# Optimization experiments

Measured on AMD Instinct MI355X. Metric: run time of the kernel, lower is better.

## Reference

```python
import jax, jax.numpy as jnp
import numpy as np

N = 50000   # num entities
R2 = 480    # num_rels * 2
D = 200     # h_dim
T = 4       # sequence_len (graph snapshots)
E = 100000  # edges per snapshot
L = 2       # rgcn layers
SLOPE = (1.0 / 8.0 + 1.0 / 3.0) / 2.0  # deterministic rrelu (eval-mode expected slope)


def setup_inputs() -> dict:
    key = jax.random.key(0)
    ks = jax.random.split(key, 13)
    s = 1.0 / np.sqrt(D)
    w = lambda k, shp, sc: jax.random.normal(k, shp, dtype=jnp.float32) * sc
    return {
        "src": jax.random.randint(ks[0], (T, E), 0, N, dtype=jnp.int32),
        "dst": jax.random.randint(ks[1], (T, E), 0, N, dtype=jnp.int32),
        "etype": jax.random.randint(ks[2], (T, E), 0, R2, dtype=jnp.int32),
        "dynamic_emb": w(ks[3], (N, D), 1.0),
        "emb_rel": w(ks[4], (R2, D), s),
        "W_ih": w(ks[5], (3 * D, 2 * D), s),
        "W_hh": w(ks[6], (3 * D, D), s),
        "b_ih": jnp.zeros((3 * D,), jnp.float32),
        "b_hh": jnp.zeros((3 * D,), jnp.float32),
        "W_neighbor": w(ks[7], (L, D, D), s),
        "W_loop": w(ks[8], (L, D, D), s),
        "time_gate_weight": w(ks[9], (D, D), s),
        "time_gate_bias": jnp.zeros((D,), jnp.float32),
    }


def _l2norm(x):
    n = jnp.linalg.norm(x, axis=-1, keepdims=True)
    return x / jnp.maximum(n, 1e-12)


def _gru(x, hprev, W_ih, W_hh, b_ih, b_hh):
    gi = x @ W_ih.T + b_ih
    gh = hprev @ W_hh.T + b_hh
    ir, iz, inn = jnp.split(gi, 3, axis=-1)
    hr, hz, hn = jnp.split(gh, 3, axis=-1)
    r = jax.nn.sigmoid(ir + hr)
    z = jax.nn.sigmoid(iz + hz)
    n = jnp.tanh(inn + r * hn)
    return (1.0 - z) * n + z * hprev


def reference(src, dst, etype, dynamic_emb, emb_rel, W_ih, W_hh, b_ih, b_hh,
              W_neighbor, W_loop, time_gate_weight, time_gate_bias):
    h_init = _l2norm(dynamic_emb)  # layer_norm=True path (F.normalize)

    def step(carry, g):
        h, h0 = carry
        s, d_, et = g
        # per-relation mean of entity embeddings touching that relation (r_to_e spans)
        ent_idx = jnp.concatenate([s, d_])          # [2E]
        seg = jnp.concatenate([et, et])             # [2E]
        ssum = jax.ops.segment_sum(h[ent_idx], seg, num_segments=R2)
        cnt = jax.ops.segment_sum(jnp.ones_like(seg, jnp.float32), seg, num_segments=R2)
        x_mean = ssum / jnp.maximum(cnt, 1.0)[:, None]          # absent rels stay 0
        x_input = jnp.concatenate([emb_rel, x_mean], axis=1)    # [R2, 2D]
        h0 = _l2norm(_gru(x_input, h0, W_ih, W_hh, b_ih, b_hh))
        # UnionRGCNLayer x L: gather -> sum-aggregate -> norm + self-loop -> rrelu
        deg = jax.ops.segment_sum(jnp.ones_like(d_, jnp.float32), d_, num_segments=N)
        norm = 1.0 / jnp.maximum(deg, 1.0)
        hh = h
        for l in range(L):
            pre = hh[s] + h0[et]                                  # [E, D]
            agg = jax.ops.segment_sum(pre, d_, num_segments=N) @ W_neighbor[l]
            out = agg * norm[:, None] + hh @ W_loop[l]
            hh = jnp.where(out >= 0, out, out * SLOPE)            # rrelu (eval)
        cur = _l2norm(hh)
        tw = jax.nn.sigmoid(h @ time_gate_weight + time_gate_bias)
        h = tw * cur + (1.0 - tw) * h
        return (h, h0), h

    (_, _), hist = jax.lax.scan(step, (h_init, emb_rel), (src, dst, etype))
    return hist  # [T, N, D] history of evolved entity embeddings
```

## Files before the change

### kernel.cpp

```cpp
#include <hip/hip_runtime.h>
#include <math.h>

#define NE 50000
#define R2C 480
#define DD 200
#define TT 4
#define EE 100000
#define SLOPE 0.22916666666666666f

#define SCCH 8
#define EPB (256 * SCCH)
#define APAD 224
#define WPAD 224
#define WSZ (208 * WPAD)
#define DCH 4096
#define DNC ((NE + DCH - 1) / DCH)
#define RSPL 8

typedef short short8 __attribute__((ext_vector_type(8)));
typedef float float4v __attribute__((ext_vector_type(4)));

__device__ __forceinline__ float sigm(float x) { return 1.f / (1.f + expf(-x)); }

__device__ __forceinline__ short f2bf(float f) {
  union { float f; unsigned u; } v;
  v.f = f;
  unsigned r = v.u + 0x7fffu + ((v.u >> 16) & 1u);
  return (short)(r >> 16);
}


__global__ void init_h_kernel(const float* __restrict__ emb, float* __restrict__ h) {
  int n = blockIdx.x;
  int lane = threadIdx.x;
  size_t base = (size_t)n * DD;
  float v0 = emb[base + lane];
  float v1 = emb[base + 64 + lane];
  float v2 = emb[base + 128 + lane];
  float v3 = (lane < 8) ? emb[base + 192 + lane] : 0.f;
  float ss = v0 * v0 + v1 * v1 + v2 * v2 + v3 * v3;
#pragma unroll
  for (int off = 32; off; off >>= 1) ss += __shfl_down(ss, off);
  ss = __shfl(ss, 0);
  float inv = 1.f / fmaxf(sqrtf(ss), 1e-12f);
  h[base + lane] = v0 * inv;
  h[base + 64 + lane] = v1 * inv;
  h[base + 128 + lane] = v2 * inv;
  if (lane < 8) h[base + 192 + lane] = v3 * inv;
}

__global__ void copy_kernel(const float* __restrict__ a, float* __restrict__ b, int n) {
  int i = blockIdx.x * blockDim.x + threadIdx.x;
  if (i < n) b[i] = a[i];
}

__global__ void fill_x_kernel(const float* __restrict__ emb_rel, float* __restrict__ X) {
  int i = blockIdx.x * blockDim.x + threadIdx.x;
  if (i >= R2C * DD) return;
  int r = i / DD, d = i - r * DD;
  X[(size_t)r * 400 + d] = emb_rel[i];
}

__global__ void prep_w_kernel(const float* __restrict__ Wnb, const float* __restrict__ Wlp,
                              const float* __restrict__ Wtg, short* __restrict__ Wb) {
  int idx = blockIdx.x * 256 + threadIdx.x;
  if (idx >= 5 * WSZ) return;
  int m = idx / WSZ, rem = idx - m * WSZ;
  int n = rem / WPAD, k = rem - n * WPAD;
  const float* s;
  if (m == 0) s = Wnb;
  else if (m == 1) s = Wnb + DD * DD;
  else if (m == 2) s = Wlp;
  else if (m == 3) s = Wlp + DD * DD;
  else s = Wtg;
  float v = (n < DD && k < DD) ? s[(size_t)k * DD + n] : 0.f;
  Wb[idx] = f2bf(v);
}

__global__ __launch_bounds__(256) void hist_kernel(const int* __restrict__ et,
                                                   const int* __restrict__ dst,
                                                   int* __restrict__ et_hist,
                                                   int* __restrict__ deg_hist) {
  __shared__ int lh[R2C];
  int t = blockIdx.y;
  int tid = threadIdx.x;
  int e0 = blockIdx.x * EPB;
  for (int i = tid; i < R2C; i += 256) lh[i] = 0;
  __syncthreads();
#pragma unroll
  for (int c = 0; c < SCCH; c++) {
    int e = e0 + c * 256 + tid;
    if (e < EE) {
      atomicAdd(&lh[et[(size_t)t * EE + e]], 1);
      atomicAdd(&deg_hist[(size_t)t * NE + dst[(size_t)t * EE + e]], 1);
    }
  }
  __syncthreads();
  for (int i = tid; i < R2C; i += 256)
    if (lh[i]) atomicAdd(&et_hist[t * R2C + i], lh[i]);
}

__global__ void scan_rel_kernel(const int* __restrict__ et_hist, int* __restrict__ rowptr) {
  int t = blockIdx.x;
  int tid = threadIdx.x;
  __shared__ int s[512];
  int v = (tid < R2C) ? 2 * et_hist[t * R2C + tid] : 0;
  s[tid] = v;
  __syncthreads();
  for (int off = 1; off < 512; off <<= 1) {
    int x = (tid >= off) ? s[tid - off] : 0;
    __syncthreads();
    s[tid] += x;
    __syncthreads();
  }
  if (tid < R2C) rowptr[t * (R2C + 1) + tid] = s[tid] - v;
  if (tid == 0) rowptr[t * (R2C + 1) + R2C] = 2 * EE;
}

__global__ __launch_bounds__(256) void deg_partial_kernel(const int* __restrict__ deg_hist,
                                                          int* __restrict__ csum) {
  int t = blockIdx.y, c = blockIdx.x, tid = threadIdx.x;
  const int* dh = deg_hist + (size_t)t * NE;
  int base = c * DCH + tid * 16;
  int s = 0;
  if (base < NE) {
    int end = base + 16 > NE ? NE : base + 16;
    for (int i = base; i < end; i++) s += dh[i];
  }
  __shared__ int red[256];
  red[tid] = s;
  __syncthreads();
  for (int off = 128; off; off >>= 1) {
    if (tid < off) red[tid] += red[tid + off];
    __syncthreads();
  }
  if (tid == 0) csum[t * DNC + c] = red[0];
}

__global__ __launch_bounds__(256) void deg_emit_kernel(const int* __restrict__ deg_hist,
                                                       const int* __restrict__ csum,
                                                       int* __restrict__ rowptr,
                                                       float* __restrict__ normv) {
  int t = blockIdx.y, c = blockIdx.x, tid = threadIdx.x;
  const int* dh = deg_hist + (size_t)t * NE;
  __shared__ int scan[256];
  __shared__ int soff;
  int base = c * DCH + tid * 16;
  int s = 0;
  if (base < NE) {
    int end = base + 16 > NE ? NE : base + 16;
    for (int i = base; i < end; i++) s += dh[i];
  }
  scan[tid] = s;
  __syncthreads();
  for (int off = 1; off < 256; off <<= 1) {
    int x = (tid >= off) ? scan[tid - off] : 0;
    __syncthreads();
    scan[tid] += x;
    __syncthreads();
  }
  if (tid == 0) {
    int o = 0;
    for (int j = 0; j < c; j++) o += csum[t * DNC + j];
    soff = o;
  }
  __syncthreads();
  int run = soff + scan[tid] - s;
  if (base < NE) {
    int end = base + 16 > NE ? NE : base + 16;
    for (int i = base; i < end; i++) {
      int v = dh[i];
      rowptr[t * (NE + 1) + i] = run;
      normv[(size_t)t * NE + i] = 1.f / fmaxf((float)v, 1.f);
      run += v;
    }
  }
  if (c == 0 && tid == 0) rowptr[t * (NE + 1) + NE] = EE;
}

__global__ __launch_bounds__(256) void scatter_rel_kernel(const int* __restrict__ src,
                                                          const int* __restrict__ dst,
                                                          const int* __restrict__ et,
                                                          const int* __restrict__ rowptr,
                                                          int* __restrict__ cursor,
                                                          int* __restrict__ sorted_ent) {
  __shared__ int lcnt[R2C];
  __shared__ int lbase[R2C];
  int t = blockIdx.y;
  int tid = threadIdx.x;
  int e0 = blockIdx.x * EPB;
  for (int i = tid; i < R2C; i += 256) lcnt[i] = 0;
  __syncthreads();
  int rels[SCCH];
#pragma unroll
  for (int c = 0; c < SCCH; c++) {
    int e = e0 + c * 256 + tid;
    int r = (e < EE) ? et[(size_t)t * EE + e] : -1;
    rels[c] = r;
    if (r >= 0) atomicAdd(&lcnt[r], 2);
  }
  __syncthreads();
  const int* rp = rowptr + t * (R2C + 1);
  for (int i = tid; i < R2C; i += 256) {
    int c = lcnt[i];
    lbase[i] = rp[i] + (c ? atomicAdd(&cursor[t * R2C + i], c) : 0);
    lcnt[i] = 0;
  }
  __syncthreads();
  int* se = sorted_ent + (size_t)t * 2 * EE;
#pragma unroll
  for (int c = 0; c < SCCH; c++) {
    int r = rels[c];
    if (r >= 0) {
      int e = e0 + c * 256 + tid;
      int off = atomicAdd(&lcnt[r], 2);
      int p = lbase[r] + off;
      se[p] = src[(size_t)t * EE + e];
      se[p + 1] = dst[(size_t)t * EE + e];
    }
  }
}

__global__ void scatter_dst_kernel(const int* __restrict__ src, const int* __restrict__ dst,
                                   const int* __restrict__ et, const int* __restrict__ rowptr,
                                   int* __restrict__ cursor, int2* __restrict__ sorted_se) {
  int i = blockIdx.x * blockDim.x + threadIdx.x;
  if (i >= TT * EE) return;
  int t = i / EE;
  int d = dst[i];
  int base = rowptr[t * (NE + 1) + d];
  int p = base + atomicAdd(&cursor[(size_t)t * NE + d], 1);
  sorted_se[(size_t)t * EE + p] = make_int2(src[i], et[i]);
}


__global__ void relmean_part_kernel(const float* __restrict__ h, const int* __restrict__ rowptr,
                                    const int* __restrict__ sorted_ent_t,
                                    float* __restrict__ Xpart) {
  int r = blockIdx.x, j = blockIdx.y;
  int beg = rowptr[r], end = rowptr[r + 1];
  int lane = threadIdx.x & 63, w = threadIdx.x >> 6;
  float a0 = 0, a1 = 0, a2 = 0, a3 = 0;
  for (int i = beg + j * 4 + w; i < end; i += 4 * RSPL) {
    int idx = sorted_ent_t[i];
    const float* row = h + (size_t)idx * DD;
    a0 += row[lane];
    a1 += row[64 + lane];
    a2 += row[128 + lane];
    if (lane < 8) a3 += row[192 + lane];
  }
  __shared__ float part[4][DD];
  part[w][lane] = a0;
  part[w][64 + lane] = a1;
  part[w][128 + lane] = a2;
  if (lane < 8) part[w][192 + lane] = a3;
  __syncthreads();
  for (int d = threadIdx.x; d < DD; d += 256) {
    Xpart[((size_t)r * RSPL + j) * DD + d] = part[0][d] + part[1][d] + part[2][d] + part[3][d];
  }
}

__global__ void relmean_comb_kernel(const float* __restrict__ Xpart,
                                    const int* __restrict__ rowptr, float* __restrict__ X) {
  int r = blockIdx.x;
  int d = threadIdx.x;
  if (d >= DD) return;
  float s = 0.f;
#pragma unroll
  for (int j = 0; j < RSPL; j++) s += Xpart[((size_t)r * RSPL + j) * DD + d];
  float cnt = fmaxf((float)(rowptr[r + 1] - rowptr[r]), 1.f);
  X[(size_t)r * 400 + 200 + d] = s / cnt;
}

__global__ __launch_bounds__(256) void gemm_gru(const float* __restrict__ X,
                                                const float* __restrict__ h0,
                                                const float* __restrict__ W_ih,
                                                const float* __restrict__ W_hh,
                                                float* __restrict__ gi) {
  int z = blockIdx.z;
  const float* A = z ? h0 : X;
  const float* B = z ? W_hh : W_ih;
  float* C = gi + (size_t)z * R2C * 600;
  int K = z ? DD : 2 * DD;
  const int M = R2C, N = 600;
  __shared__ float As[32][33];
  __shared__ float Bs[32][33];
  int tid = threadIdx.x;
  int col0 = blockIdx.x * 32;
  int row0 = blockIdx.y * 32;
  int tr = tid >> 4, tc = tid & 15;
  float a00 = 0, a01 = 0, a10 = 0, a11 = 0;
  for (int k0 = 0; k0 < K; k0 += 32) {
    __syncthreads();
    for (int i = tid; i < 1024; i += 256) {
      int kk = i & 31, r = i >> 5;
      int row = row0 + r, k = k0 + kk;
      As[kk][r] = (row < M && k < K) ? A[(size_t)row * K + k] : 0.f;
    }
    for (int i = tid; i < 1024; i += 256) {
      int kk = i & 31, c = i >> 5;
      int col = col0 + c, k = k0 + kk;
      Bs[kk][c] = (col < N && k < K) ? B[(size_t)col * K + k] : 0.f;
    }
    __syncthreads();
#pragma unroll
    for (int kk = 0; kk < 32; kk++) {
      float x0 = As[kk][tr * 2], x1 = As[kk][tr * 2 + 1];
      float y0 = Bs[kk][tc * 2], y1 = Bs[kk][tc * 2 + 1];
      a00 += x0 * y0;
      a01 += x0 * y1;
      a10 += x1 * y0;
      a11 += x1 * y1;
    }
  }
  int row = row0 + tr * 2, col = col0 + tc * 2;
  if (row < M && col < N) C[(size_t)row * N + col] = a00;
  if (row < M && col + 1 < N) C[(size_t)row * N + col + 1] = a01;
  if (row + 1 < M && col < N) C[(size_t)(row + 1) * N + col] = a10;
  if (row + 1 < M && col + 1 < N) C[(size_t)(row + 1) * N + col + 1] = a11;
}

__global__ void gru_gate_kernel(const float* __restrict__ gi, const float* __restrict__ gh,
                                const float* __restrict__ b_ih, const float* __restrict__ b_hh,
                                float* __restrict__ h0) {
  int r = blockIdx.x;
  int tid = threadIdx.x;
  int lane = tid & 63, w = tid >> 6;
  __shared__ float red[4];
  float o = 0.f;
  if (tid < DD) {
    size_t b = (size_t)r * (3 * DD);
    float ir = gi[b + tid] + b_ih[tid];
    float iz = gi[b + DD + tid] + b_ih[DD + tid];
    float inn = gi[b + 2 * DD + tid] + b_ih[2 * DD + tid];
    float hr = gh[b + tid] + b_hh[tid];
    float hz = gh[b + DD + tid] + b_hh[DD + tid];
    float hn = gh[b + 2 * DD + tid] + b_hh[2 * DD + tid];
    float hv = h0[(size_t)r * DD + tid];
    float rr = sigm(ir + hr);
    float z = sigm(iz + hz);
    float n = tanhf(inn + rr * hn);
    o = (1.f - z) * n + z * hv;
  }
  float ss = o * o;
#pragma unroll
  for (int off = 32; off; off >>= 1) ss += __shfl_down(ss, off);
  if (lane == 0) red[w] = ss;
  __syncthreads();
  float tot = red[0] + red[1] + red[2] + red[3];
  float inv = 1.f / fmaxf(sqrtf(tot), 1e-12f);
  if (tid < DD) h0[(size_t)r * DD + tid] = o * inv;
}

__global__ void agg_kernel(const float* __restrict__ hh, const float* __restrict__ h0,
                           const int* __restrict__ rowptr, const int2* __restrict__ se_t,
                           const float* __restrict__ normv_t, short* __restrict__ aggb) {
  int w = threadIdx.x >> 6, lane = threadIdx.x & 63;
  int n = blockIdx.x * 4 + w;
  if (n >= NE) return;
  int beg = rowptr[n], end = rowptr[n + 1];
  float a0 = 0, a1 = 0, a2 = 0, a3 = 0;
  for (int i = beg; i < end; i++) {
    int2 p = se_t[i];
    const float* hr = hh + (size_t)p.x * DD;
    const float* qr = h0 + (size_t)p.y * DD;
    a0 += hr[lane] + qr[lane];
    a1 += hr[64 + lane] + qr[64 + lane];
    a2 += hr[128 + lane] + qr[128 + lane];
    if (lane < 8) a3 += hr[192 + lane] + qr[192 + lane];
  }
  float nm = normv_t[n];
  short* outp = aggb + (size_t)n * APAD;
  outp[lane] = f2bf(a0 * nm);
  outp[64 + lane] = f2bf(a1 * nm);
  outp[128 + lane] = f2bf(a2 * nm);
  if (lane < 8) outp[192 + lane] = f2bf(a3 * nm);
  else if (lane < 32) outp[192 + lane] = 0;
}


__global__ __launch_bounds__(256) void gemm_dual(const short* __restrict__ A1,
                                                 const short* __restrict__ Wb1,
                                                 const float* __restrict__ A2,
                                                 const short* __restrict__ Wb2,
                                                 float* __restrict__ C) {
  __shared__ short Bt[2][208][40];
  int tid = threadIdx.x;
  int lane = tid & 63, w = tid >> 6;
  int quad = lane >> 4, l16 = lane & 15;
  int row = blockIdx.x * 64 + w * 16 + l16;
  bool rok = row < NE;

  short8 af1[7], af2[7];
#pragma unroll
  for (int c = 0; c < 7; c++) {
    af1[c] = rok ? *(const short8*)(A1 + (size_t)row * APAD + c * 32 + quad * 8)
                 : (short8){0, 0, 0, 0, 0, 0, 0, 0};
  }
#pragma unroll
  for (int c = 0; c < 7; c++) {
    int kb = c * 32 + quad * 8;
    short8 a = (short8){0, 0, 0, 0, 0, 0, 0, 0};
    if (rok && kb < DD) {
      const float* ap = A2 + (size_t)row * DD + kb;
      float4v v0 = *(const float4v*)ap;
      float4v v1 = *(const float4v*)(ap + 4);
      short tmp[8] = {f2bf(v0[0]), f2bf(v0[1]), f2bf(v0[2]), f2bf(v0[3]),
                      f2bf(v1[0]), f2bf(v1[1]), f2bf(v1[2]), f2bf(v1[3])};
      a = *(short8*)&tmp[0];
    }
    af2[c] = a;
  }

  float4v acc[13];
#pragma unroll
  for (int ct = 0; ct < 13; ct++) acc[ct] = (float4v){0.f, 0.f, 0.f, 0.f};

#pragma unroll
  for (int c = 0; c < 7; c++) {
    __syncthreads();
#pragma unroll
    for (int it = 0; it < 7; it++) {
      int s = tid + it * 256;
      if (s < 1664) {
        int m = s >= 832;
        int ss = s - m * 832;
        int n = ss % 208, k8 = (ss / 208) * 8;
        const short* Wb = m ? Wb2 : Wb1;
        *(short8*)&Bt[m][n][k8] = *(const short8*)&Wb[(size_t)n * WPAD + c * 32 + k8];
      }
    }
    __syncthreads();
#pragma unroll
    for (int ct = 0; ct < 13; ct++) {
      short8 b1 = *(short8*)&Bt[0][ct * 16 + l16][quad * 8];
      short8 b2 = *(short8*)&Bt[1][ct * 16 + l16][quad * 8];
      acc[ct] = __builtin_amdgcn_mfma_f32_16x16x32_bf16(af1[c], b1, acc[ct], 0, 0, 0);
      acc[ct] = __builtin_amdgcn_mfma_f32_16x16x32_bf16(af2[c], b2, acc[ct], 0, 0, 0);
    }
  }
  int r0 = blockIdx.x * 64 + w * 16 + quad * 4;
#pragma unroll
  for (int ct = 0; ct < 13; ct++) {
    int col = ct * 16 + l16;
    if (col >= DD) continue;
#pragma unroll
    for (int i = 0; i < 4; i++) {
      int r = r0 + i;
      if (r < NE) {
        float v = acc[ct][i];
        v = (v >= 0.f) ? v : v * SLOPE;
        C[(size_t)r * DD + col] = v;
      }
    }
  }
}

__global__ __launch_bounds__(256) void gemm_tgfin(const float* __restrict__ A,
                                                  const short* __restrict__ Wb,
                                                  const float* __restrict__ hh,
                                                  const float* __restrict__ tgb,
                                                  float* __restrict__ outp) {
  __shared__ short Bt[208][40];
  int tid = threadIdx.x;
  int lane = tid & 63, w = tid >> 6;
  int quad = lane >> 4, l16 = lane & 15;
  int row = blockIdx.x * 64 + w * 16 + l16;
  bool rok = row < NE;

  short8 af[7];
#pragma unroll
  for (int c = 0; c < 7; c++) {
    int kb = c * 32 + quad * 8;
    short8 a = (short8){0, 0, 0, 0, 0, 0, 0, 0};
    if (rok && kb < DD) {
      const float* ap = A + (size_t)row * DD + kb;
      float4v v0 = *(const float4v*)ap;
      float4v v1 = *(const float4v*)(ap + 4);
      short tmp[8] = {f2bf(v0[0]), f2bf(v0[1]), f2bf(v0[2]), f2bf(v0[3]),
                      f2bf(v1[0]), f2bf(v1[1]), f2bf(v1[2]), f2bf(v1[3])};
      a = *(short8*)&tmp[0];
    }
    af[c] = a;
  }

  float4v acc[13];
#pragma unroll
  for (int ct = 0; ct < 13; ct++) acc[ct] = (float4v){0.f, 0.f, 0.f, 0.f};

#pragma unroll
  for (int c = 0; c < 7; c++) {
    __syncthreads();
#pragma unroll
    for (int it = 0; it < 4; it++) {
      int s = tid + it * 256;
      if (s < 832) {
        int n = s % 208, k8 = (s / 208) * 8;
        *(short8*)&Bt[n][k8] = *(const short8*)&Wb[(size_t)n * WPAD + c * 32 + k8];
      }
    }
    __syncthreads();
#pragma unroll
    for (int ct = 0; ct < 13; ct++) {
      short8 bf = *(short8*)&Bt[ct * 16 + l16][quad * 8];
      acc[ct] = __builtin_amdgcn_mfma_f32_16x16x32_bf16(af[c], bf, acc[ct], 0, 0, 0);
    }
  }
  int rbase = blockIdx.x * 64 + w * 16 + quad * 4;
#pragma unroll
  for (int i = 0; i < 4; i++) {
    int r = rbase + i;
    bool ok = r < NE;
    size_t rb = (size_t)r * DD;
    float ssq = 0.f;
#pragma unroll
    for (int ct = 0; ct < 13; ct++) {
      int col = ct * 16 + l16;
      float x = (ok && col < DD) ? hh[rb + col] : 0.f;
      ssq += x * x;
    }
#pragma unroll
    for (int off = 1; off < 16; off <<= 1) ssq += __shfl_xor(ssq, off);
    float inv = 1.f / fmaxf(sqrtf(ssq), 1e-12f);
#pragma unroll
    for (int ct = 0; ct < 13; ct++) {
      int col = ct * 16 + l16;
      if (ok && col < DD) {
        float cur = hh[rb + col] * inv;
        float tw = sigm(acc[ct][i] + tgb[col]);
        outp[rb + col] = tw * cur + (1.f - tw) * A[rb + col];
      }
    }
  }
}


extern "C" void kernel_launch(void* const* d_in, const int* in_sizes, int n_in, void* d_out,
                              int out_size, void* d_ws, size_t ws_size, hipStream_t stream) {
  const int* src = (const int*)d_in[0];
  const int* dst = (const int*)d_in[1];
  const int* et = (const int*)d_in[2];
  const float* dyn = (const float*)d_in[3];
  const float* emb_rel = (const float*)d_in[4];
  const float* W_ih = (const float*)d_in[5];
  const float* W_hh = (const float*)d_in[6];
  const float* b_ih = (const float*)d_in[7];
  const float* b_hh = (const float*)d_in[8];
  const float* W_nb = (const float*)d_in[9];
  const float* W_lp = (const float*)d_in[10];
  const float* Wtg = (const float*)d_in[11];
  const float* tgb = (const float*)d_in[12];
  float* out = (float*)d_out;

  char* p = (char*)d_ws;
  float* h = (float*)p;        p += (size_t)NE * DD * 4;
  float* bufB = (float*)p;     p += (size_t)NE * DD * 4;
  float* agg = (float*)p;      p += (size_t)NE * DD * 4;
  float* h0 = (float*)p;       p += (size_t)R2C * DD * 4;
  float* X = (float*)p;        p += (size_t)R2C * 400 * 4;
  float* normv = (float*)p;    p += (size_t)TT * NE * 4;
  int* et_rowptr = (int*)p;    p += (size_t)TT * (R2C + 1) * 4;
  int* et_cursor = (int*)p;    p += (size_t)TT * R2C * 4;
  int* et_hist = (int*)p;      p += (size_t)TT * R2C * 4;
  int* sorted_ent = (int*)p;   p += (size_t)TT * 2 * EE * 4;
  int* dst_rowptr = (int*)p;   p += (size_t)TT * (NE + 1) * 4;
  int* dst_cursor = (int*)p;   p += (size_t)TT * NE * 4;
  int* deg_hist = (int*)p;     p += (size_t)TT * NE * 4;
  int2* sorted_se = (int2*)p;  p += (size_t)TT * EE * 8;
  short* Wb = (short*)p;       p += (size_t)5 * WSZ * 2;
  float* Xpart = (float*)p;    p += (size_t)R2C * RSPL * DD * 4;
  int* csum = (int*)p;         p += (size_t)TT * DNC * 4;

  float* gi = bufB;
  float* gh = bufB + (size_t)R2C * 3 * DD;
  short* aggb = (short*)agg;

  hipMemsetAsync(et_hist, 0, (size_t)TT * R2C * 4, stream);
  hipMemsetAsync(deg_hist, 0, (size_t)TT * NE * 4, stream);
  hipMemsetAsync(et_cursor, 0, (size_t)TT * R2C * 4, stream);
  hipMemsetAsync(dst_cursor, 0, (size_t)TT * NE * 4, stream);

  init_h_kernel<<<NE, 64, 0, stream>>>(dyn, h);
  copy_kernel<<<(R2C * DD + 255) / 256, 256, 0, stream>>>(emb_rel, h0, R2C * DD);
  fill_x_kernel<<<(R2C * DD + 255) / 256, 256, 0, stream>>>(emb_rel, X);
  prep_w_kernel<<<(5 * WSZ + 255) / 256, 256, 0, stream>>>(W_nb, W_lp, Wtg, Wb);
  const dim3 bin_grid((EE + EPB - 1) / EPB, TT);
  hist_kernel<<<bin_grid, 256, 0, stream>>>(et, dst, et_hist, deg_hist);
  scan_rel_kernel<<<TT, 512, 0, stream>>>(et_hist, et_rowptr);
  const dim3 deg_grid(DNC, TT);
  deg_partial_kernel<<<deg_grid, 256, 0, stream>>>(deg_hist, csum);
  deg_emit_kernel<<<deg_grid, 256, 0, stream>>>(deg_hist, csum, dst_rowptr, normv);
  scatter_rel_kernel<<<bin_grid, 256, 0, stream>>>(src, dst, et, et_rowptr, et_cursor, sorted_ent);
  scatter_dst_kernel<<<(TT * EE + 255) / 256, 256, 0, stream>>>(src, dst, et, dst_rowptr,
                                                                dst_cursor, sorted_se);

  const int gemm_grid = (NE + 63) / 64;
  const dim3 gru_grid((600 + 31) / 32, (R2C + 31) / 32, 2);
  const dim3 rm_grid(R2C, RSPL);
  for (int t = 0; t < TT; t++) {
    const float* hcur = (t == 0) ? h : out + (size_t)(t - 1) * NE * DD;
    float* bufA = out + (size_t)t * NE * DD;

    relmean_part_kernel<<<rm_grid, 256, 0, stream>>>(hcur, et_rowptr + t * (R2C + 1),
                                                     sorted_ent + (size_t)t * 2 * EE, Xpart);
    relmean_comb_kernel<<<R2C, 256, 0, stream>>>(Xpart, et_rowptr + t * (R2C + 1), X);
    gemm_gru<<<gru_grid, 256, 0, stream>>>(X, h0, W_ih, W_hh, gi);
    gru_gate_kernel<<<R2C, 256, 0, stream>>>(gi, gh, b_ih, b_hh, h0);
    agg_kernel<<<(NE + 3) / 4, 256, 0, stream>>>(hcur, h0, dst_rowptr + t * (NE + 1),
                                                 sorted_se + (size_t)t * EE,
                                                 normv + (size_t)t * NE, aggb);
    gemm_dual<<<gemm_grid, 256, 0, stream>>>(aggb, Wb + 0 * WSZ, hcur, Wb + 2 * WSZ, bufA);
    agg_kernel<<<(NE + 3) / 4, 256, 0, stream>>>(bufA, h0, dst_rowptr + t * (NE + 1),
                                                 sorted_se + (size_t)t * EE,
                                                 normv + (size_t)t * NE, aggb);
    gemm_dual<<<gemm_grid, 256, 0, stream>>>(aggb, Wb + 1 * WSZ, bufA, Wb + 3 * WSZ, bufB);
    gemm_tgfin<<<gemm_grid, 256, 0, stream>>>(hcur, Wb + 4 * WSZ, bufB, tgb, bufA);
  }
}
```

Baseline: 1.435 ms.

## Fuse time-gate GEMM into layer-0 GEMM and finalize in layer-1 epilogue

The time-gate GEMM on the current embedding now runs inside the layer-0 dual GEMM, because both use the same A operand (hcur). Its pre-activation output is written to a scratch buffer. The layer-1 GEMM now does the L2 normalization, sigmoid gate and blend directly from its accumulator registers. This removes one kernel launch per step, one write and read of the full layer-1 output, and a second conversion of hcur to bf16. In exchange, the layer-0 kernel holds twice as many accumulators and more shared memory, which can lower occupancy. The layer-1 kernel also writes its result back into the same buffer it read as input.

```diff
diff --git a/kernel.cpp b/kernel.cpp
--- a/kernel.cpp
+++ b/kernel.cpp
@@ -379,12 +379,13 @@
 }
 
 
-__global__ __launch_bounds__(256) void gemm_dual(const short* __restrict__ A1,
-                                                 const short* __restrict__ Wb1,
-                                                 const float* __restrict__ A2,
-                                                 const short* __restrict__ Wb2,
-                                                 float* __restrict__ C) {
-  __shared__ short Bt[2][208][40];
+__global__ __launch_bounds__(256) void gemm_l0(const short* __restrict__ A1,
+                                               const float* __restrict__ A2,
+                                               const short* __restrict__ WbN,
+                                               const short* __restrict__ WbL,
+                                               const short* __restrict__ WbT,
+                                               float* __restrict__ C, float* __restrict__ tg) {
+  __shared__ short Bt[3][208][40];
   int tid = threadIdx.x;
   int lane = tid & 63, w = tid >> 6;
   int quad = lane >> 4, l16 = lane & 15;
@@ -412,6 +413,92 @@
     af2[c] = a;
   }
 
+  float4v accA[13], accT[13];
+#pragma unroll
+  for (int ct = 0; ct < 13; ct++) {
+    accA[ct] = (float4v){0.f, 0.f, 0.f, 0.f};
+    accT[ct] = (float4v){0.f, 0.f, 0.f, 0.f};
+  }
+
+#pragma unroll
+  for (int c = 0; c < 7; c++) {
+    __syncthreads();
+#pragma unroll
+    for (int it = 0; it < 10; it++) {
+      int s = tid + it * 256;
+      if (s < 2496) {
+        int m = s / 832;
+        int ss = s - m * 832;
+        int n = ss % 208, k8 = (ss / 208) * 8;
+        const short* Wb = (m == 0) ? WbN : (m == 1) ? WbL : WbT;
+        *(short8*)&Bt[m][n][k8] = *(const short8*)&Wb[(size_t)n * WPAD + c * 32 + k8];
+      }
+    }
+    __syncthreads();
+#pragma unroll
+    for (int ct = 0; ct < 13; ct++) {
+      short8 b0 = *(short8*)&Bt[0][ct * 16 + l16][quad * 8];
+      short8 b1 = *(short8*)&Bt[1][ct * 16 + l16][quad * 8];
+      short8 b2 = *(short8*)&Bt[2][ct * 16 + l16][quad * 8];
+      accA[ct] = __builtin_amdgcn_mfma_f32_16x16x32_bf16(af1[c], b0, accA[ct], 0, 0, 0);
+      accA[ct] = __builtin_amdgcn_mfma_f32_16x16x32_bf16(af2[c], b1, accA[ct], 0, 0, 0);
+      accT[ct] = __builtin_amdgcn_mfma_f32_16x16x32_bf16(af2[c], b2, accT[ct], 0, 0, 0);
+    }
+  }
+  int r0 = blockIdx.x * 64 + w * 16 + quad * 4;
+#pragma unroll
+  for (int ct = 0; ct < 13; ct++) {
+    int col = ct * 16 + l16;
+    if (col >= DD) continue;
+#pragma unroll
+    for (int i = 0; i < 4; i++) {
+      int r = r0 + i;
+      if (r < NE) {
+        float v = accA[ct][i];
+        v = (v >= 0.f) ? v : v * SLOPE;
+        C[(size_t)r * DD + col] = v;
+        tg[(size_t)r * DD + col] = accT[ct][i];
+      }
+    }
+  }
+}
+
+__global__ __launch_bounds__(256) void gemm_l1(const short* __restrict__ A1,
+                                               const float* __restrict__ A2,
+                                               const short* __restrict__ WbN,
+                                               const short* __restrict__ WbL,
+                                               const float* __restrict__ tg,
+                                               const float* __restrict__ tgb,
+                                               const float* __restrict__ hcur,
+                                               float* __restrict__ outp) {
+  __shared__ short Bt[2][208][40];
+  int tid = threadIdx.x;
+  int lane = tid & 63, w = tid >> 6;
+  int quad = lane >> 4, l16 = lane & 15;
+  int row = blockIdx.x * 64 + w * 16 + l16;
+  bool rok = row < NE;
+
+  short8 af1[7], af2[7];
+#pragma unroll
+  for (int c = 0; c < 7; c++) {
+    af1[c] = rok ? *(const short8*)(A1 + (size_t)row * APAD + c * 32 + quad * 8)
+                 : (short8){0, 0, 0, 0, 0, 0, 0, 0};
+  }
+#pragma unroll
+  for (int c = 0; c < 7; c++) {
+    int kb = c * 32 + quad * 8;
+    short8 a = (short8){0, 0, 0, 0, 0, 0, 0, 0};
+    if (rok && kb < DD) {
+      const float* ap = A2 + (size_t)row * DD + kb;
+      float4v v0 = *(const float4v*)ap;
+      float4v v1 = *(const float4v*)(ap + 4);
+      short tmp[8] = {f2bf(v0[0]), f2bf(v0[1]), f2bf(v0[2]), f2bf(v0[3]),
+                      f2bf(v1[0]), f2bf(v1[1]), f2bf(v1[2]), f2bf(v1[3])};
+      a = *(short8*)&tmp[0];
+    }
+    af2[c] = a;
+  }
+
   float4v acc[13];
 #pragma unroll
   for (int ct = 0; ct < 13; ct++) acc[ct] = (float4v){0.f, 0.f, 0.f, 0.f};
@@ -426,7 +513,7 @@
         int m = s >= 832;
         int ss = s - m * 832;
         int n = ss % 208, k8 = (ss / 208) * 8;
-        const short* Wb = m ? Wb2 : Wb1;
+        const short* Wb = m ? WbL : WbN;
         *(short8*)&Bt[m][n][k8] = *(const short8*)&Wb[(size_t)n * WPAD + c * 32 + k8];
       }
     }
@@ -439,73 +526,13 @@
       acc[ct] = __builtin_amdgcn_mfma_f32_16x16x32_bf16(af2[c], b2, acc[ct], 0, 0, 0);
     }
   }
-  int r0 = blockIdx.x * 64 + w * 16 + quad * 4;
-#pragma unroll
-  for (int ct = 0; ct < 13; ct++) {
-    int col = ct * 16 + l16;
-    if (col >= DD) continue;
+#pragma unroll
+  for (int ct = 0; ct < 13; ct++)
 #pragma unroll
     for (int i = 0; i < 4; i++) {
-      int r = r0 + i;
-      if (r < NE) {
-        float v = acc[ct][i];
-        v = (v >= 0.f) ? v : v * SLOPE;
-        C[(size_t)r * DD + col] = v;
-      }
-    }
-  }
-}
-
-__global__ __launch_bounds__(256) void gemm_tgfin(const float* __restrict__ A,
-                                                  const short* __restrict__ Wb,
-                                                  const float* __restrict__ hh,
-                                                  const float* __restrict__ tgb,
-                                                  float* __restrict__ outp) {
-  __shared__ short Bt[208][40];
-  int tid = threadIdx.x;
-  int lane = tid & 63, w = tid >> 6;
-  int quad = lane >> 4, l16 = lane & 15;
-  int row = blockIdx.x * 64 + w * 16 + l16;
-  bool rok = row < NE;
-
-  short8 af[7];
-#pragma unroll
-  for (int c = 0; c < 7; c++) {
-    int kb = c * 32 + quad * 8;
-    short8 a = (short8){0, 0, 0, 0, 0, 0, 0, 0};
-    if (rok && kb < DD) {
-      const float* ap = A + (size_t)row * DD + kb;
-      float4v v0 = *(const float4v*)ap;
-      float4v v1 = *(const float4v*)(ap + 4);
-      short tmp[8] = {f2bf(v0[0]), f2bf(v0[1]), f2bf(v0[2]), f2bf(v0[3]),
-                      f2bf(v1[0]), f2bf(v1[1]), f2bf(v1[2]), f2bf(v1[3])};
-      a = *(short8*)&tmp[0];
-    }
-    af[c] = a;
-  }
-
-  float4v acc[13];
-#pragma unroll
-  for (int ct = 0; ct < 13; ct++) acc[ct] = (float4v){0.f, 0.f, 0.f, 0.f};
-
-#pragma unroll
-  for (int c = 0; c < 7; c++) {
-    __syncthreads();
-#pragma unroll
-    for (int it = 0; it < 4; it++) {
-      int s = tid + it * 256;
-      if (s < 832) {
-        int n = s % 208, k8 = (s / 208) * 8;
-        *(short8*)&Bt[n][k8] = *(const short8*)&Wb[(size_t)n * WPAD + c * 32 + k8];
-      }
-    }
-    __syncthreads();
-#pragma unroll
-    for (int ct = 0; ct < 13; ct++) {
-      short8 bf = *(short8*)&Bt[ct * 16 + l16][quad * 8];
-      acc[ct] = __builtin_amdgcn_mfma_f32_16x16x32_bf16(af[c], bf, acc[ct], 0, 0, 0);
-    }
-  }
+      float v = acc[ct][i];
+      acc[ct][i] = (v >= 0.f) ? v : v * SLOPE;
+    }
   int rbase = blockIdx.x * 64 + w * 16 + quad * 4;
 #pragma unroll
   for (int i = 0; i < 4; i++) {
@@ -515,8 +542,7 @@
     float ssq = 0.f;
 #pragma unroll
     for (int ct = 0; ct < 13; ct++) {
-      int col = ct * 16 + l16;
-      float x = (ok && col < DD) ? hh[rb + col] : 0.f;
+      float x = acc[ct][i];
       ssq += x * x;
     }
 #pragma unroll
@@ -526,9 +552,9 @@
     for (int ct = 0; ct < 13; ct++) {
       int col = ct * 16 + l16;
       if (ok && col < DD) {
-        float cur = hh[rb + col] * inv;
-        float tw = sigm(acc[ct][i] + tgb[col]);
-        outp[rb + col] = tw * cur + (1.f - tw) * A[rb + col];
+        float cur = acc[ct][i] * inv;
+        float tw = sigm(tg[rb + col] + tgb[col]);
+        outp[rb + col] = tw * cur + (1.f - tw) * hcur[rb + col];
       }
     }
   }
@@ -574,6 +600,7 @@
   float* gi = bufB;
   float* gh = bufB + (size_t)R2C * 3 * DD;
   short* aggb = (short*)agg;
+  float* tg = bufB;
 
   hipMemsetAsync(et_hist, 0, (size_t)TT * R2C * 4, stream);
   hipMemsetAsync(deg_hist, 0, (size_t)TT * NE * 4, stream);
@@ -609,11 +636,12 @@
     agg_kernel<<<(NE + 3) / 4, 256, 0, stream>>>(hcur, h0, dst_rowptr + t * (NE + 1),
                                                  sorted_se + (size_t)t * EE,
                                                  normv + (size_t)t * NE, aggb);
-    gemm_dual<<<gemm_grid, 256, 0, stream>>>(aggb, Wb + 0 * WSZ, hcur, Wb + 2 * WSZ, bufA);
+    gemm_l0<<<gemm_grid, 256, 0, stream>>>(aggb, hcur, Wb + 0 * WSZ, Wb + 2 * WSZ, Wb + 4 * WSZ,
+                                           bufA, tg);
     agg_kernel<<<(NE + 3) / 4, 256, 0, stream>>>(bufA, h0, dst_rowptr + t * (NE + 1),
                                                  sorted_se + (size_t)t * EE,
                                                  normv + (size_t)t * NE, aggb);
-    gemm_dual<<<gemm_grid, 256, 0, stream>>>(aggb, Wb + 1 * WSZ, bufA, Wb + 3 * WSZ, bufB);
-    gemm_tgfin<<<gemm_grid, 256, 0, stream>>>(hcur, Wb + 4 * WSZ, bufB, tgb, bufA);
-  }
-}
+    gemm_l1<<<gemm_grid, 256, 0, stream>>>(aggb, bufA, Wb + 1 * WSZ, Wb + 3 * WSZ, tg, tgb, hcur,
+                                           bufA);
+  }
+}
```

After: 1.494 ms. 1.04x slower.
